# Optimization experiments

Measured on AMD Instinct MI355X. Metric: run time of the kernel, lower is better.

Reference implementation:

```python
import jax, jax.numpy as jnp
import numpy as np

N_NODES = 50000
N_EDGES = 1_600_000
Q_MULT = 8          # charges_irreps = 8x0e
NODE_MULT = 64      # node_feat_irreps = 64x0e + 64x1o
RBF = 8             # edge_feats_irreps num_irreps
HID = 64            # FullyConnectedNet hidden width
W_NUMEL = 2 * Q_MULT  # edge_tp weight_numel: two uvu paths (0e->0e, 0e x 1o->1o), u=8


def setup_inputs() -> dict:
    key = jax.random.key(0)
    k = jax.random.split(key, 14)
    f = lambda kk, sh: jax.random.normal(kk, sh, dtype=jnp.float32)
    return {
        "node_feats": f(k[0], (N_NODES, NODE_MULT * 4)),          # 64 scalars + 64 vectors(3)
        "charges_0": f(k[1], (N_NODES, Q_MULT)),                  # unused in forward
        "charges_induced": f(k[2], (N_NODES, Q_MULT)),
        "edge_feats": f(k[3], (N_EDGES, RBF)),
        "edge_attrs": f(k[4], (N_EDGES, 4)),                      # Y0 (1) + Y1 (3)
        "field_feats": f(k[5], (N_NODES, RBF)),                   # unused in forward
        "mlp_w1": f(k[6], (RBF, HID)),
        "mlp_w2": f(k[7], (HID, HID)),
        "mlp_w3": f(k[8], (HID, HID)),
        "mlp_w4": f(k[9], (HID, W_NUMEL)),
        "W0": f(k[10], (Q_MULT, NODE_MULT)),                      # node_tp path 0e x 0e -> 0e
        "W1": f(k[11], (Q_MULT, NODE_MULT)),                      # node_tp path 1o x 1o -> 0e
        "edge_index": jax.random.randint(k[12], (2, N_EDGES), 0, N_NODES, dtype=jnp.int32),
        "batch": jnp.zeros((N_NODES,), dtype=jnp.int32),
    }


def reference(node_feats, charges_0, charges_induced, edge_feats, edge_attrs,
              field_feats, mlp_w1, mlp_w2, mlp_w3, mlp_w4, W0, W1,
              edge_index, batch):
    sender, receiver = edge_index[0], edge_index[1]
    num_nodes = node_feats.shape[0]

    # e3nn FullyConnectedNet: variance-normalized linear layers + silu
    h = edge_feats
    for w in (mlp_w1, mlp_w2, mlp_w3):
        h = jax.nn.silu(h @ (w / np.sqrt(np.float32(w.shape[0]))))
    tp_w = h @ (mlp_w4 / np.sqrt(np.float32(mlp_w4.shape[0])))   # [E, 16]
    w0, w1 = tp_w[:, :Q_MULT], tp_w[:, Q_MULT:]                   # per-edge path weights

    # edge_tp (uvu, external weights): gather sender charges, weighted CG product
    q_s = charges_induced[sender]                                  # [E, 8]
    mid0 = (w0 * q_s) * edge_attrs[:, :1]                          # [E, 8]    0e
    mid1 = (w1 * q_s)[:, :, None] * edge_attrs[:, None, 1:4]       # [E, 8, 3] 1o

    # scatter-sum messages to receiver nodes
    sum0 = jax.ops.segment_sum(mid0, receiver, num_segments=num_nodes)
    sum1 = jax.ops.segment_sum(mid1.reshape(-1, Q_MULT * 3), receiver,
                               num_segments=num_nodes).reshape(-1, Q_MULT, 3)

    # node_tp: FullyConnectedTensorProduct(8x0e+8x1o, 64x0e+64x1o -> 1x0e)
    node0 = node_feats[:, :NODE_MULT]                              # [N, 64]
    node1 = node_feats[:, NODE_MULT:].reshape(-1, NODE_MULT, 3)    # [N, 64, 3]
    c = 1.0 / np.sqrt(np.float32(Q_MULT * NODE_MULT * 2))          # path normalization
    e0 = jnp.einsum('nu,nv,uv->n', sum0, node0, W0)
    e1 = jnp.einsum('nuk,nvk,uv->n', sum1, node1, W1) / np.sqrt(np.float32(3.0))  # w3j(1,1,0)
    return c * (e0 + e1)                                           # [N] per-node energy
```

## Files before the change

### kernel.cpp

```cpp
#include <hip/hip_runtime.h>
#include <hip/hip_bf16.h>

typedef short short8 __attribute__((ext_vector_type(8)));
typedef float f32x4 __attribute__((ext_vector_type(4)));

#define EW 12

static __device__ __forceinline__ float bf2f(unsigned int b) { return __uint_as_float(b << 16); }
static __device__ __forceinline__ short fb2s(float x) {
    unsigned u = __float_as_uint(x);
    return (short)((u + 0x7FFFu + ((u >> 16) & 1u)) >> 16);
}
static __device__ __forceinline__ short fb2s_fast(float x) {
    return (short)((__float_as_uint(x) + 0x8000u) >> 16);
}
static __device__ __forceinline__ float silu(float x) {
    return x * __builtin_amdgcn_rcpf(1.0f + __expf(-x));
}
static __device__ __forceinline__ float load1(const void* p, long off, int isbf) {
    return isbf ? bf2f(((const unsigned short*)p)[off]) : ((const float*)p)[off];
}
static __device__ __forceinline__ void load4(const void* p, long off, int isbf, float* o) {
    if (isbf) {
        uint2 v = *(const uint2*)((const unsigned short*)p + off);
        o[0]=bf2f(v.x&0xffffu); o[1]=bf2f(v.x>>16);
        o[2]=bf2f(v.y&0xffffu); o[3]=bf2f(v.y>>16);
    } else {
        float4 v = *(const float4*)((const float*)p + off);
        o[0]=v.x; o[1]=v.y; o[2]=v.z; o[3]=v.w;
    }
}
static __device__ __forceinline__ int detect_bf16(const void* nf) {
    const unsigned int* w = (const unsigned int*)nf;
    int lane = threadIdx.x & 63;
    unsigned int e = (w[lane] >> 7) & 0xFFu;
    unsigned long long m = __ballot(e >= 118u && e <= 132u);
    return __popcll(m) >= 32 ? 1 : 0;
}

#define NB 32
__global__ __launch_bounds__(256) void k_node(
    const void* __restrict__ nf, const void* __restrict__ W0, const void* __restrict__ W1,
    const void* __restrict__ w1, const void* __restrict__ w2,
    const void* __restrict__ w3, const void* __restrict__ w4,
    short* __restrict__ Bws, float* __restrict__ NA, float* __restrict__ acc, int n_nodes) {
    __shared__ float Nd0[NB * 68];
    __shared__ float Nd1[3 * NB * 68];
    __shared__ float W0L[8 * 68];
    __shared__ float W1L[8 * 68];
    const int tid = threadIdx.x;
    const int isbf = detect_bf16(nf);
    const long n0 = (long)blockIdx.x * NB;

    if (blockIdx.x < 44) {
        int idx = blockIdx.x * 256 + tid;
        int j = idx & 7, lane = (idx >> 3) & 63, tile = idx >> 9;
        int n16 = lane & 15, kq = lane >> 4;
        float v;
        if (tile < 4) {
            int k = kq * 8 + j, n = tile * 16 + n16;
            v = (k < 8) ? load1(w1, k * 64 + n, isbf) : 0.0f;
        } else if (tile < 12) {
            int t = (tile - 4) >> 1, kt = (tile - 4) & 1;
            int k = kt * 32 + kq * 8 + j, n = t * 16 + n16;
            v = load1(w2, k * 64 + n, isbf) * 0.125f;
        } else if (tile < 20) {
            int t = (tile - 12) >> 1, kt = (tile - 12) & 1;
            int k = kt * 32 + kq * 8 + j, n = t * 16 + n16;
            v = load1(w3, k * 64 + n, isbf) * 0.125f;
        } else {
            int kt = tile - 20;
            int k = kt * 32 + kq * 8 + j, n = n16;
            v = load1(w4, k * 16 + n, isbf) * 0.125f;
        }
        Bws[idx] = fb2s(v);
    }
    if (tid < NB) {
        long n = n0 + tid;
        if (n < n_nodes) acc[n] = 0.0f;
    }
    if (n0 >= n_nodes) return;

    for (int i = tid; i < 512; i += 256) {
        W0L[(i >> 6) * 68 + (i & 63)] = load1(W0, i, isbf);
        W1L[(i >> 6) * 68 + (i & 63)] = load1(W1, i, isbf);
    }
    if (isbf) {
        for (int i = tid; i < NB * 32; i += 256) {
            int node = i >> 5, c8 = (i & 31) * 8;
            long ng = n0 + node; if (ng > n_nodes - 1) ng = n_nodes - 1;
            uint4 v = *(const uint4*)((const unsigned short*)nf + ng * 256 + c8);
            float f[8];
            f[0]=bf2f(v.x&0xffffu); f[1]=bf2f(v.x>>16);
            f[2]=bf2f(v.y&0xffffu); f[3]=bf2f(v.y>>16);
            f[4]=bf2f(v.z&0xffffu); f[5]=bf2f(v.z>>16);
            f[6]=bf2f(v.w&0xffffu); f[7]=bf2f(v.w>>16);
            #pragma unroll
            for (int t = 0; t < 8; t++) {
                int col = c8 + t;
                if (col < 64) Nd0[node * 68 + col] = f[t];
                else {
                    int cc = col - 64, vv = cc / 3, kk = cc - vv * 3;
                    Nd1[(kk * NB + node) * 68 + vv] = f[t];
                }
            }
        }
    } else {
        for (int i = tid; i < NB * 64; i += 256) {
            int node = i >> 6, c4 = (i & 63) * 4;
            long ng = n0 + node; if (ng > n_nodes - 1) ng = n_nodes - 1;
            float4 v = *(const float4*)((const float*)nf + ng * 256 + c4);
            float f[4] = {v.x, v.y, v.z, v.w};
            #pragma unroll
            for (int t = 0; t < 4; t++) {
                int col = c4 + t;
                if (col < 64) Nd0[node * 68 + col] = f[t];
                else {
                    int cc = col - 64, vv = cc / 3, kk = cc - vv * 3;
                    Nd1[(kk * NB + node) * 68 + vv] = f[t];
                }
            }
        }
    }
    __syncthreads();

    const int wv = tid >> 6, lane = tid & 63;
    const int u = lane & 7, ln = lane >> 3;
    float sum[4] = {0.0f, 0.0f, 0.0f, 0.0f};

    if (wv == 0) {
        const float* w = &W0L[u * 68];
        for (int v0 = 0; v0 < 64; v0 += 4) {
            float4 w4 = *(const float4*)(w + v0);
            #pragma unroll
            for (int j = 0; j < 4; j++) {
                float4 nd = *(const float4*)&Nd0[(ln + 8 * j) * 68 + v0];
                sum[j] += w4.x * nd.x + w4.y * nd.y + w4.z * nd.z + w4.w * nd.w;
            }
        }
        #pragma unroll
        for (int j = 0; j < 4; j++) {
            long node = n0 + ln + 8 * j;
            if (node < n_nodes) NA[node * 32 + u] = sum[j] * 0.03125f;
        }
    } else {
        const int kk = wv - 1;
        const float* w = &W1L[u * 68];
        const float* nd1 = &Nd1[kk * NB * 68];
        for (int v0 = 0; v0 < 64; v0 += 4) {
            float4 w4 = *(const float4*)(w + v0);
            #pragma unroll
            for (int j = 0; j < 4; j++) {
                float4 nd = *(const float4*)&nd1[(ln + 8 * j) * 68 + v0];
                sum[j] += w4.x * nd.x + w4.y * nd.y + w4.z * nd.z + w4.w * nd.w;
            }
        }
        #pragma unroll
        for (int j = 0; j < 4; j++) {
            long node = n0 + ln + 8 * j;
            if (node < n_nodes) NA[node * 32 + 8 + u * 3 + kk] = sum[j] * 0.018042195912175804f;
        }
    }
}

__global__ __launch_bounds__(EW * 64) void k_edges_mfma(
    const void* __restrict__ ef, const void* __restrict__ ea, const void* __restrict__ qc,
    const int* __restrict__ eidx, const void* __restrict__ nf,
    const short* __restrict__ Bws, const float* __restrict__ NA,
    float* __restrict__ acc, int n_edges) {
    __shared__ short W[11264];
    __shared__ short Hs[EW * 2304];
    const int tid = threadIdx.x, lane = tid & 63, wv = tid >> 6;
    const int n16 = lane & 15, kq = lane >> 4;
    const int isbf = detect_bf16(nf);

    {
        const uint4* src = (const uint4*)Bws;
        uint4* dst = (uint4*)W;
        for (int i = tid; i < 1408; i += EW * 64) dst[i] = src[i];
    }
    __syncthreads();

    const long E0 = (long)blockIdx.x * (EW * 32) + wv * 32;
    short* Hw = Hs + wv * 2304;

    int woff[4];
    #pragma unroll
    for (int t = 0; t < 4; t++)
        woff[t] = (((t * 2 + (n16 >> 3)) ^ (kq >> 1)) << 3) + (n16 & 7);
    const int rbit = (n16 >> 3) & 1;

    short8 a1[2];
    #pragma unroll
    for (int mt = 0; mt < 2; mt++) {
        short8 a = {0,0,0,0,0,0,0,0};
        if (kq == 0) {
            long e = E0 + mt * 16 + n16;
            if (e > n_edges - 1) e = n_edges - 1;
            if (isbf) {
                a = *(const short8*)((const unsigned short*)ef + e * 8);
            } else {
                const float* pe = (const float*)ef + e * 8;
                float4 v0 = *(const float4*)pe, v1 = *(const float4*)(pe + 4);
                a[0]=fb2s(v0.x); a[1]=fb2s(v0.y); a[2]=fb2s(v0.z); a[3]=fb2s(v0.w);
                a[4]=fb2s(v1.x); a[5]=fb2s(v1.y); a[6]=fb2s(v1.z); a[7]=fb2s(v1.w);
            }
        }
        a1[mt] = a;
    }

    const f32x4 zero = {0.0f, 0.0f, 0.0f, 0.0f};

    {
        f32x4 c1[2][4];
        #pragma unroll
        for (int t = 0; t < 4; t++) {
            short8 b = *(const short8*)(W + t * 512 + lane * 8);
            #pragma unroll
            for (int mt = 0; mt < 2; mt++)
                c1[mt][t] = __builtin_amdgcn_mfma_f32_16x16x32_bf16(a1[mt], b, zero, 0, 0, 0);
        }
        #pragma unroll
        for (int mt = 0; mt < 2; mt++)
            #pragma unroll
            for (int t = 0; t < 4; t++)
                #pragma unroll
                for (int r = 0; r < 4; r++) {
                    float v = silu(c1[mt][t][r] * 0.35355339059327373f);
                    Hw[(mt * 16 + kq * 4 + r) * 72 + woff[t]] = fb2s_fast(v);
                }
    }

    #pragma unroll
    for (int L = 0; L < 2; L++) {
        const int base = (L == 0) ? 4 : 12;
        short8 a[2][2];
        #pragma unroll
        for (int mt = 0; mt < 2; mt++)
            #pragma unroll
            for (int kt = 0; kt < 2; kt++)
                a[mt][kt] = *(const short8*)(Hw + (mt * 16 + n16) * 72 + (((kt * 4 + kq) ^ rbit) << 3));
        f32x4 c2[2][4];
        #pragma unroll
        for (int mt = 0; mt < 2; mt++)
            #pragma unroll
            for (int t = 0; t < 4; t++) c2[mt][t] = zero;
        #pragma unroll
        for (int kt = 0; kt < 2; kt++)
            #pragma unroll
            for (int t = 0; t < 4; t++) {
                short8 b = *(const short8*)(W + (base + t * 2 + kt) * 512 + lane * 8);
                #pragma unroll
                for (int mt = 0; mt < 2; mt++)
                    c2[mt][t] = __builtin_amdgcn_mfma_f32_16x16x32_bf16(a[mt][kt], b, c2[mt][t], 0, 0, 0);
            }
        #pragma unroll
        for (int mt = 0; mt < 2; mt++)
            #pragma unroll
            for (int t = 0; t < 4; t++)
                #pragma unroll
                for (int r = 0; r < 4; r++) {
                    float v = silu(c2[mt][t][r]);
                    Hw[(mt * 16 + kq * 4 + r) * 72 + woff[t]] = fb2s_fast(v);
                }
    }

    float* TP = (float*)Hw;
    {
        short8 a[2][2];
        #pragma unroll
        for (int mt = 0; mt < 2; mt++)
            #pragma unroll
            for (int kt = 0; kt < 2; kt++)
                a[mt][kt] = *(const short8*)(Hw + (mt * 16 + n16) * 72 + (((kt * 4 + kq) ^ rbit) << 3));
        f32x4 c4[2] = {zero, zero};
        #pragma unroll
        for (int kt = 0; kt < 2; kt++) {
            short8 b = *(const short8*)(W + (20 + kt) * 512 + lane * 8);
            #pragma unroll
            for (int mt = 0; mt < 2; mt++)
                c4[mt] = __builtin_amdgcn_mfma_f32_16x16x32_bf16(a[mt][kt], b, c4[mt], 0, 0, 0);
        }
        #pragma unroll
        for (int mt = 0; mt < 2; mt++)
            #pragma unroll
            for (int r = 0; r < 4; r++)
                TP[(mt * 16 + kq * 4 + r) * 20 + n16] = c4[mt][r];
    }

    {
        const int el = lane >> 1, h = lane & 1;
        const long e = E0 + el;
        long ec = e;
        if (ec > n_edges - 1) ec = n_edges - 1;
        const int s = eidx[ec];
        const int r = eidx[(long)n_edges + ec];

        float4 t0 = *(const float4*)(TP + el * 20 + h * 4);
        float4 t1 = *(const float4*)(TP + el * 20 + 8 + h * 4);
        float tp0[4] = {t0.x, t0.y, t0.z, t0.w};
        float tp1[4] = {t1.x, t1.y, t1.z, t1.w};

        float q[4];
        load4(qc, (long)s * 8 + h * 4, isbf, q);
        float eav[4];
        load4(ea, ec * 4, isbf, eav);

        const float* nr = NA + (long)r * 32;
        float4 n0 = *(const float4*)(nr + h * 4);
        float t12[12];
        *(float4*)(t12 + 0) = *(const float4*)(nr + 8 + h * 12);
        *(float4*)(t12 + 4) = *(const float4*)(nr + 12 + h * 12);
        *(float4*)(t12 + 8) = *(const float4*)(nr + 16 + h * 12);

        float n0a[4] = {n0.x, n0.y, n0.z, n0.w};
        float p = 0.0f;
        #pragma unroll
        for (int i = 0; i < 4; i++) {
            float d = eav[1] * t12[i * 3] + eav[2] * t12[i * 3 + 1] + eav[3] * t12[i * 3 + 2];
            p += tp0[i] * q[i] * eav[0] * n0a[i] + tp1[i] * q[i] * d;
        }
        p += __shfl_xor(p, 1);
        if (h == 0 && e < n_edges) atomicAdd(&acc[r], p);
    }
}

__global__ void k_out(const float* __restrict__ acc, void* __restrict__ out,
                      const void* __restrict__ nf, int n) {
    const int isbf = detect_bf16(nf);
    int i = blockIdx.x * 256 + threadIdx.x;
    if (i >= n) return;
    if (isbf) ((__hip_bfloat16*)out)[i] = __float2bfloat16(acc[i]);
    else      ((float*)out)[i] = acc[i];
}

extern "C" void kernel_launch(void* const* d_in, const int* in_sizes, int n_in,
                              void* d_out, int out_size, void* d_ws, size_t ws_size,
                              hipStream_t stream) {
    const void* node_feats      = d_in[0];
    const void* charges_induced = d_in[2];
    const void* edge_feats      = d_in[3];
    const void* edge_attrs      = d_in[4];
    const void* mlp_w1          = d_in[6];
    const void* mlp_w2          = d_in[7];
    const void* mlp_w3          = d_in[8];
    const void* mlp_w4          = d_in[9];
    const void* W0              = d_in[10];
    const void* W1              = d_in[11];
    const int*  edge_index      = (const int*)d_in[12];

    const int n_nodes = in_sizes[0] / 256;
    const int n_edges = in_sizes[3] / 8;

    short* Bws = (short*)d_ws;
    float* NA  = (float*)((char*)d_ws + 22528);
    float* acc = NA + (size_t)n_nodes * 32;

    int nblk = (n_nodes + NB - 1) / NB;
    if (nblk < 44) nblk = 44;
    k_node<<<nblk, 256, 0, stream>>>(node_feats, W0, W1,
        mlp_w1, mlp_w2, mlp_w3, mlp_w4, Bws, NA, acc, n_nodes);
    const int epb = EW * 32;
    k_edges_mfma<<<(n_edges + epb - 1) / epb, EW * 64, 0, stream>>>(
        edge_feats, edge_attrs, charges_induced, edge_index, node_feats, Bws, NA, acc, n_edges);
    k_out<<<(n_nodes + 255) / 256, 256, 0, stream>>>(acc, d_out, node_feats, n_nodes);
}
```

Baseline: 364.8 us.

## Read MLP weights from global, shrink blocks, hoist gather loads early

The edge kernel no longer stages the MLP weight fragments into shared memory behind a barrier. Each wave now reads the B fragments directly from global memory, relying on cache hits. Blocks shrink from 12 waves to 4 with a launch-bounds occupancy hint, which cuts shared memory per block. The edge-index, charge, edge-attribute and node-aggregate gathers are issued before the MLP so their latency overlaps the MFMA work, at the cost of more live registers.

```diff
diff --git a/kernel.cpp b/kernel.cpp
--- a/kernel.cpp
+++ b/kernel.cpp
@@ -4,7 +4,7 @@
 typedef short short8 __attribute__((ext_vector_type(8)));
 typedef float f32x4 __attribute__((ext_vector_type(4)));
 
-#define EW 12
+#define EW 4
 
 static __device__ __forceinline__ float bf2f(unsigned int b) { return __uint_as_float(b << 16); }
 static __device__ __forceinline__ short fb2s(float x) {
@@ -163,23 +163,15 @@
     }
 }
 
-__global__ __launch_bounds__(EW * 64) void k_edges_mfma(
+__global__ __launch_bounds__(256, 6) void k_edges_mfma(
     const void* __restrict__ ef, const void* __restrict__ ea, const void* __restrict__ qc,
     const int* __restrict__ eidx, const void* __restrict__ nf,
     const short* __restrict__ Bws, const float* __restrict__ NA,
     float* __restrict__ acc, int n_edges) {
-    __shared__ short W[11264];
     __shared__ short Hs[EW * 2304];
     const int tid = threadIdx.x, lane = tid & 63, wv = tid >> 6;
     const int n16 = lane & 15, kq = lane >> 4;
     const int isbf = detect_bf16(nf);
-
-    {
-        const uint4* src = (const uint4*)Bws;
-        uint4* dst = (uint4*)W;
-        for (int i = tid; i < 1408; i += EW * 64) dst[i] = src[i];
-    }
-    __syncthreads();
 
     const long E0 = (long)blockIdx.x * (EW * 32) + wv * 32;
     short* Hw = Hs + wv * 2304;
@@ -189,6 +181,14 @@
     for (int t = 0; t < 4; t++)
         woff[t] = (((t * 2 + (n16 >> 3)) ^ (kq >> 1)) << 3) + (n16 & 7);
     const int rbit = (n16 >> 3) & 1;
+
+    const int el = lane >> 1, h = lane & 1;
+    const long e_ep = E0 + el;
+    long ec = e_ep; if (ec > n_edges - 1) ec = n_edges - 1;
+    const int s = eidx[ec];
+    const int r = eidx[(long)n_edges + ec];
+    float q[4];   load4(qc, (long)s * 8 + h * 4, isbf, q);
+    float eav[4]; load4(ea, ec * 4, isbf, eav);
 
     short8 a1[2];
     #pragma unroll
@@ -215,7 +215,7 @@
         f32x4 c1[2][4];
         #pragma unroll
         for (int t = 0; t < 4; t++) {
-            short8 b = *(const short8*)(W + t * 512 + lane * 8);
+            short8 b = *(const short8*)(Bws + t * 512 + lane * 8);
             #pragma unroll
             for (int mt = 0; mt < 2; mt++)
                 c1[mt][t] = __builtin_amdgcn_mfma_f32_16x16x32_bf16(a1[mt], b, zero, 0, 0, 0);
@@ -225,9 +225,9 @@
             #pragma unroll
             for (int t = 0; t < 4; t++)
                 #pragma unroll
-                for (int r = 0; r < 4; r++) {
-                    float v = silu(c1[mt][t][r] * 0.35355339059327373f);
-                    Hw[(mt * 16 + kq * 4 + r) * 72 + woff[t]] = fb2s_fast(v);
+                for (int r2 = 0; r2 < 4; r2++) {
+                    float v = silu(c1[mt][t][r2] * 0.35355339059327373f);
+                    Hw[(mt * 16 + kq * 4 + r2) * 72 + woff[t]] = fb2s_fast(v);
                 }
     }
 
@@ -249,7 +249,7 @@
         for (int kt = 0; kt < 2; kt++)
             #pragma unroll
             for (int t = 0; t < 4; t++) {
-                short8 b = *(const short8*)(W + (base + t * 2 + kt) * 512 + lane * 8);
+                short8 b = *(const short8*)(Bws + (base + t * 2 + kt) * 512 + lane * 8);
                 #pragma unroll
                 for (int mt = 0; mt < 2; mt++)
                     c2[mt][t] = __builtin_amdgcn_mfma_f32_16x16x32_bf16(a[mt][kt], b, c2[mt][t], 0, 0, 0);
@@ -259,11 +259,18 @@
             #pragma unroll
             for (int t = 0; t < 4; t++)
                 #pragma unroll
-                for (int r = 0; r < 4; r++) {
-                    float v = silu(c2[mt][t][r]);
-                    Hw[(mt * 16 + kq * 4 + r) * 72 + woff[t]] = fb2s_fast(v);
+                for (int r2 = 0; r2 < 4; r2++) {
+                    float v = silu(c2[mt][t][r2]);
+                    Hw[(mt * 16 + kq * 4 + r2) * 72 + woff[t]] = fb2s_fast(v);
                 }
     }
+
+    const float* nr = NA + (long)r * 32;
+    float4 n0 = *(const float4*)(nr + h * 4);
+    float t12[12];
+    *(float4*)(t12 + 0) = *(const float4*)(nr + 8 + h * 12);
+    *(float4*)(t12 + 4) = *(const float4*)(nr + 12 + h * 12);
+    *(float4*)(t12 + 8) = *(const float4*)(nr + 16 + h * 12);
 
     float* TP = (float*)Hw;
     {
@@ -276,7 +283,7 @@
         f32x4 c4[2] = {zero, zero};
         #pragma unroll
         for (int kt = 0; kt < 2; kt++) {
-            short8 b = *(const short8*)(W + (20 + kt) * 512 + lane * 8);
+            short8 b = *(const short8*)(Bws + (20 + kt) * 512 + lane * 8);
             #pragma unroll
             for (int mt = 0; mt < 2; mt++)
                 c4[mt] = __builtin_amdgcn_mfma_f32_16x16x32_bf16(a[mt][kt], b, c4[mt], 0, 0, 0);
@@ -284,35 +291,15 @@
         #pragma unroll
         for (int mt = 0; mt < 2; mt++)
             #pragma unroll
-            for (int r = 0; r < 4; r++)
-                TP[(mt * 16 + kq * 4 + r) * 20 + n16] = c4[mt][r];
+            for (int r2 = 0; r2 < 4; r2++)
+                TP[(mt * 16 + kq * 4 + r2) * 20 + n16] = c4[mt][r2];
     }
 
     {
-        const int el = lane >> 1, h = lane & 1;
-        const long e = E0 + el;
-        long ec = e;
-        if (ec > n_edges - 1) ec = n_edges - 1;
-        const int s = eidx[ec];
-        const int r = eidx[(long)n_edges + ec];
-
         float4 t0 = *(const float4*)(TP + el * 20 + h * 4);
         float4 t1 = *(const float4*)(TP + el * 20 + 8 + h * 4);
         float tp0[4] = {t0.x, t0.y, t0.z, t0.w};
         float tp1[4] = {t1.x, t1.y, t1.z, t1.w};
-
-        float q[4];
-        load4(qc, (long)s * 8 + h * 4, isbf, q);
-        float eav[4];
-        load4(ea, ec * 4, isbf, eav);
-
-        const float* nr = NA + (long)r * 32;
-        float4 n0 = *(const float4*)(nr + h * 4);
-        float t12[12];
-        *(float4*)(t12 + 0) = *(const float4*)(nr + 8 + h * 12);
-        *(float4*)(t12 + 4) = *(const float4*)(nr + 12 + h * 12);
-        *(float4*)(t12 + 8) = *(const float4*)(nr + 16 + h * 12);
-
         float n0a[4] = {n0.x, n0.y, n0.z, n0.w};
         float p = 0.0f;
         #pragma unroll
@@ -321,7 +308,7 @@
             p += tp0[i] * q[i] * eav[0] * n0a[i] + tp1[i] * q[i] * d;
         }
         p += __shfl_xor(p, 1);
-        if (h == 0 && e < n_edges) atomicAdd(&acc[r], p);
+        if (h == 0 && e_ep < n_edges) atomicAdd(&acc[r], p);
     }
 }
 
```

Result: slower. 543.9 us (+49.1%).
